# Performance work log

Measured on AMD Instinct MI355X. Metric: run time of the kernel, lower is better.

The kernel has to match this reference:

```python
import jax, jax.numpy as jnp
import numpy as np

N_NODES = 50000
K_MAX = 10
BATCH = 64
T = 32
N_INPUTS = 16
BITS_PER_FEATURE = 4
INPUT_BITS = N_INPUTS * BITS_PER_FEATURE  # 64


def setup_inputs() -> dict:
    key = jax.random.key(0)
    ks = jax.random.split(key, 8)
    x = jax.random.randint(ks[0], (BATCH, T, INPUT_BITS), 0, 2, dtype=jnp.int32)
    adj_list = jax.random.randint(ks[1], (N_NODES, K_MAX), 0, N_NODES, dtype=jnp.int32)
    adj_list_mask = jax.random.randint(ks[2], (N_NODES, K_MAX), 0, 2, dtype=jnp.int32)
    lut = jax.random.randint(ks[3], (N_NODES, 2 ** K_MAX), 0, 2, dtype=jnp.int32)
    init_states = jax.random.randint(ks[4], (N_NODES,), 0, 2, dtype=jnp.int32)
    input_nodes = jax.random.randint(ks[5], (INPUT_BITS,), 0, N_NODES, dtype=jnp.int32)
    W = jax.random.normal(ks[6], (N_INPUTS, N_NODES), dtype=jnp.float32) * (1.0 / np.sqrt(N_NODES))
    b = jax.random.normal(ks[7], (N_INPUTS,), dtype=jnp.float32) * 0.01
    return {"x": x, "adj_list": adj_list, "adj_list_mask": adj_list_mask,
            "lut": lut, "init_states": init_states, "input_nodes": input_nodes,
            "W": W, "b": b}


def reference(x, adj_list, adj_list_mask, lut, init_states, input_nodes, W, b):
    B, T_, _ = x.shape
    N, K = adj_list.shape
    # powers_of_2 = 2**arange(K).flip()  (MSB-first bit packing)
    pow2 = (2 ** jnp.arange(K - 1, -1, -1)).astype(jnp.int32)  # [K]
    node_ids = jnp.arange(N, dtype=jnp.int32)  # [N]
    s0 = jnp.broadcast_to(init_states[None, :], (B, N)).astype(jnp.int32)

    def step(states, x_t):
        # xor input perturbation at input_nodes
        cur = states[:, input_nodes]                      # [B, INPUT_BITS]
        states = states.at[:, input_nodes].set(jnp.bitwise_xor(cur, x_t))
        # gather masked neighbor states and bit-pack into LUT index
        neigh = jnp.take(states, adj_list, axis=1)        # [B, N, K]
        idx = jnp.sum(neigh * adj_list_mask[None] * pow2, axis=-1)  # [B, N]
        new_states = lut[node_ids[None, :], idx]          # [B, N]
        return new_states, None

    final_states, _ = jax.lax.scan(step, s0, jnp.moveaxis(x, 1, 0))
    # readout = nn.Linear(n_nodes, n_inputs) on final binary states
    out = final_states.astype(jnp.float32) @ W.T + b      # [B, N_INPUTS]
    return out
```

## Files before the change

### kernel.cpp

```cpp
#include <hip/hip_runtime.h>
#include <stdint.h>

#define N_NODES    50000
#define K_MAX      10
#define BATCH      64
#define T_STEPS    32
#define N_INPUTS   16
#define INPUT_BITS 64

#define NPW   224
#define NWG   224
#define NTHR  896
#define GRPN  14
#define GRP_SZ 16
#define NBUF  (T_STEPS + 1)

#define BUF_STRIDE_B 400128u

#define OFF_BUFS   0u
#define OFF_XMASK  13204224u
#define OFF_GCTR   13220608u
#define OFF_RCTR   13335296u
#define OFF_PLUT   13343488u

__global__ void prep_kernel(const int* __restrict__ x,
                            const int* __restrict__ init_states,
                            const int* __restrict__ input_nodes,
                            uint64_t* __restrict__ bufs,
                            uint64_t* __restrict__ xmask,
                            uint32_t* __restrict__ gctr,
                            uint32_t* __restrict__ rctr) {
    const int gid = blockIdx.x * blockDim.x + threadIdx.x;
    const size_t strw = BUF_STRIDE_B / 8;
    if (gid < N_NODES) {
        int n = gid;
        int jm = -1;
        for (int j = 0; j < INPUT_BITS; ++j)
            if (input_nodes[j] == n) jm = j;
        uint64_t v = init_states[n] ? ~0ull : 0ull;
        if (jm >= 0) {
            uint64_t m = 0ull;
            for (int b = 0; b < BATCH; ++b)
                m |= (uint64_t)(x[b * (T_STEPS * INPUT_BITS) + jm] & 1) << b;
            v ^= m;
        }
        bufs[n] = v;
    } else if (gid < N_NODES + NBUF) {
        bufs[(size_t)(gid - N_NODES) * strw + N_NODES] = 0ull;
    } else if (gid < N_NODES + NBUF + T_STEPS * INPUT_BITS) {
        int k = gid - (N_NODES + NBUF);
        int t = k >> 6, j = k & 63;
        uint64_t m = 0ull;
        for (int b = 0; b < BATCH; ++b)
            m |= (uint64_t)(x[b * (T_STEPS * INPUT_BITS) + t * INPUT_BITS + j] & 1) << b;
        xmask[k] = m;
    } else {
        int c = gid - (N_NODES + NBUF + T_STEPS * INPUT_BITS);
        if (c < T_STEPS * GRPN) gctr[c * 64] = 0;
        else if (c < T_STEPS * GRPN + T_STEPS)
            rctr[(c - T_STEPS * GRPN) * 64] = 0;
    }
}

__global__ void lutpack_kernel(const int* __restrict__ lut,
                               uint64_t* __restrict__ plut) {
    const int tid = threadIdx.x;
    const int blk = blockIdx.x;
    const int lane = tid & 63, wave = tid >> 6;
    int v = lut[(size_t)blk * 1024 + tid];
    uint64_t m = __ballot(v & 1);
    if (lane == 0) plut[(size_t)blk * 16 + wave] = m;
}

__global__ __launch_bounds__(NTHR)
void reservoir_coop(const uint64_t* __restrict__ plut,
                    const int* __restrict__ adj,
                    const int* __restrict__ adjmask,
                    const int* __restrict__ input_nodes,
                    const uint64_t* __restrict__ xmask,
                    uint64_t* __restrict__ bufs,
                    uint32_t* __restrict__ gctr,
                    uint32_t* __restrict__ rctr) {
    __shared__ uint8_t lutb[NPW * 128];

    const int tid = threadIdx.x;
    const int wg  = blockIdx.x;
    const int grp = wg >> 4;

    {
        const uint4* s = (const uint4*)(plut + (size_t)wg * NPW * 16);
        uint4* d = (uint4*)lutb;
        d[tid]        = s[tid];
        d[tid + NTHR] = s[tid + NTHR];
    }

    const int nl   = tid >> 2;
    const int q    = tid & 3;
    const int node = wg * NPW + nl;
    const bool valid = node < N_NODES;
    const uint32_t qsh = (uint32_t)(q & 1) * 16;

    uint32_t off[K_MAX];
    uint32_t soff = 0;
    int jm = -1;
    if (valid) {
        #pragma unroll
        for (int k = 0; k < K_MAX; ++k) {
            int a  = adj[node * K_MAX + k];
            int mk = adjmask[node * K_MAX + k];
            off[k] = (uint32_t)(mk ? a : N_NODES) * 8u + (uint32_t)(q >> 1) * 4u;
        }
        for (int j = 0; j < INPUT_BITS; ++j)
            if (input_nodes[j] == node) jm = j;
        soff = (uint32_t)node * 8u + (uint32_t)(q >> 1) * 4u;
    }
    const uint32_t* lut32 = (const uint32_t*)lutb;
    const uint32_t* xm32  = (const uint32_t*)xmask;
    const int rowbase = nl * 32;
    __syncthreads();

    for (int t = 0; t < T_STEPS; ++t) {
        const char* src = (const char*)bufs + (size_t)t * BUF_STRIDE_B;
        char*       dst = (char*)bufs + (size_t)(t + 1) * BUF_STRIDE_B;
        if (valid) {
            uint32_t w[K_MAX];
            #pragma unroll
            for (int k = 0; k < K_MAX; ++k)
                w[k] = *(const uint32_t*)(src + off[k]) >> qsh;

            uint32_t o16 = 0;
            #pragma unroll
            for (int b = 0; b < 16; ++b) {
                uint32_t idx = 0;
                #pragma unroll
                for (int k = 0; k < K_MAX; ++k)
                    idx = (idx << 1) | ((w[k] >> b) & 1u);
                uint32_t d = lut32[rowbase + (idx >> 5)];
                o16 |= ((d >> (idx & 31)) & 1u) << b;
            }

            uint32_t hi = __shfl_down(o16, 1);
            if ((q & 1) == 0) {
                uint32_t o32 = o16 | (hi << 16);
                if (jm >= 0 && t < T_STEPS - 1)
                    o32 ^= xm32[((t + 1) * INPUT_BITS + jm) * 2 + (q >> 1)];
                __hip_atomic_store((uint32_t*)(dst + soff), o32,
                                   __ATOMIC_RELAXED, __HIP_MEMORY_SCOPE_AGENT);
            }
        }

        if (t < T_STEPS - 1) {
            __syncthreads();
            if (tid == 0) {
                uint32_t* gc = gctr + ((size_t)t * GRPN + grp) * 64;
                uint32_t* rc = rctr + (size_t)t * 64;
                uint32_t old = __hip_atomic_fetch_add(gc, 1u, __ATOMIC_RELAXED,
                                                      __HIP_MEMORY_SCOPE_AGENT);
                if (old == GRP_SZ - 1)
                    __hip_atomic_fetch_add(rc, 1u, __ATOMIC_RELAXED,
                                           __HIP_MEMORY_SCOPE_AGENT);
                while (__hip_atomic_load(rc, __ATOMIC_RELAXED, __HIP_MEMORY_SCOPE_AGENT)
                       < (uint32_t)GRPN)
                    __builtin_amdgcn_s_sleep(1);
            }
            __syncthreads();
        }
    }
}

__global__ void out_kernel(const uint64_t* __restrict__ fstate,
                           const float* __restrict__ W,
                           const float* __restrict__ bias,
                           float* __restrict__ out) {
    const int wg = blockIdx.x;
    const int b = wg >> 4, i = wg & 15;
    const int tid = threadIdx.x;
    const uint8_t* st = (const uint8_t*)fstate;
    const int byteoff = b >> 3, bsh = b & 7;

    float s = 0.f;
    for (int n = tid; n < N_NODES; n += 256) {
        uint32_t bit = (st[(size_t)n * 8 + byteoff] >> bsh) & 1u;
        s += (float)bit * W[(size_t)i * N_NODES + n];
    }
    #pragma unroll
    for (int off = 32; off; off >>= 1) s += __shfl_down(s, off);

    __shared__ float part[4];
    const int lane = tid & 63, wave = tid >> 6;
    if (lane == 0) part[wave] = s;
    __syncthreads();
    if (tid == 0) out[wg] = part[0] + part[1] + part[2] + part[3] + bias[i];
}

extern "C" void kernel_launch(void* const* d_in, const int* in_sizes, int n_in,
                              void* d_out, int out_size, void* d_ws, size_t ws_size,
                              hipStream_t stream) {
    const int*   x       = (const int*)d_in[0];
    const int*   adj     = (const int*)d_in[1];
    const int*   adjmask = (const int*)d_in[2];
    const int*   lut     = (const int*)d_in[3];
    const int*   initst  = (const int*)d_in[4];
    const int*   innodes = (const int*)d_in[5];
    const float* W       = (const float*)d_in[6];
    const float* bias    = (const float*)d_in[7];
    float* out = (float*)d_out;

    char* ws = (char*)d_ws;
    uint64_t* bufs  = (uint64_t*)(ws + OFF_BUFS);
    uint64_t* xmask = (uint64_t*)(ws + OFF_XMASK);
    uint32_t* gctr  = (uint32_t*)(ws + OFF_GCTR);
    uint32_t* rctr  = (uint32_t*)(ws + OFF_RCTR);
    uint64_t* plut  = (uint64_t*)(ws + OFF_PLUT);

    {
        int prep_threads = N_NODES + NBUF + T_STEPS * INPUT_BITS
                         + T_STEPS * GRPN + T_STEPS;
        int prep_blocks = (prep_threads + 255) / 256;
        hipLaunchKernelGGL(prep_kernel, dim3(prep_blocks), dim3(256), 0, stream,
                           x, initst, innodes, bufs, xmask, gctr, rctr);
    }

    hipLaunchKernelGGL(lutpack_kernel, dim3(N_NODES), dim3(1024), 0, stream, lut, plut);

    {
        void* args[] = { (void*)&plut, (void*)&adj, (void*)&adjmask, (void*)&innodes,
                         (void*)&xmask, (void*)&bufs, (void*)&gctr, (void*)&rctr };
        hipLaunchCooperativeKernel((void*)reservoir_coop,
                                   dim3(NWG), dim3(NTHR),
                                   args, 0, stream);
    }

    hipLaunchKernelGGL(out_kernel, dim3(BATCH * N_INPUTS), dim3(256), 0, stream,
                       (const uint64_t*)(ws + OFF_BUFS + (size_t)T_STEPS * BUF_STRIDE_B),
                       W, bias, out);
}
```

Before: 365.0 us.

## Fuse LUT bit-packing into cooperative kernel and regrid to 512 smaller workgroups

Removes the separate lutpack kernel and its packed-LUT round trip through global memory. Each workgroup now ballots its own nodes' int32 LUT rows straight into shared memory. The cooperative grid changes from 224 workgroups of 896 threads to 512 of 448 threads, which spreads the one-time 200 MB LUT read across more CUs and raises the number of barrier groups. The cost is more participants in every per-step grid barrier. Threads beyond NPW now run the compute on dummy offsets and skip only the store.

After: 384.2 us. 5.3% more time.

```diff
diff --git a/kernel.cpp b/kernel.cpp
--- a/kernel.cpp
+++ b/kernel.cpp
@@ -8,10 +8,10 @@
 #define N_INPUTS   16
 #define INPUT_BITS 64
 
-#define NPW   224
-#define NWG   224
-#define NTHR  896
-#define GRPN  14
+#define NPW   98
+#define NWG   512
+#define NTHR  448
+#define GRPN  32
 #define GRP_SZ 16
 #define NBUF  (T_STEPS + 1)
 
@@ -20,8 +20,7 @@
 #define OFF_BUFS   0u
 #define OFF_XMASK  13204224u
 #define OFF_GCTR   13220608u
-#define OFF_RCTR   13335296u
-#define OFF_PLUT   13343488u
+#define OFF_RCTR   13482752u
 
 __global__ void prep_kernel(const int* __restrict__ x,
                             const int* __restrict__ init_states,
@@ -62,20 +61,10 @@
     }
 }
 
-__global__ void lutpack_kernel(const int* __restrict__ lut,
-                               uint64_t* __restrict__ plut) {
-    const int tid = threadIdx.x;
-    const int blk = blockIdx.x;
-    const int lane = tid & 63, wave = tid >> 6;
-    int v = lut[(size_t)blk * 1024 + tid];
-    uint64_t m = __ballot(v & 1);
-    if (lane == 0) plut[(size_t)blk * 16 + wave] = m;
-}
-
 __global__ __launch_bounds__(NTHR)
-void reservoir_coop(const uint64_t* __restrict__ plut,
-                    const int* __restrict__ adj,
+void reservoir_coop(const int* __restrict__ adj,
                     const int* __restrict__ adjmask,
+                    const int* __restrict__ lut,
                     const int* __restrict__ input_nodes,
                     const uint64_t* __restrict__ xmask,
                     uint64_t* __restrict__ bufs,
@@ -83,26 +72,39 @@
                     uint32_t* __restrict__ rctr) {
     __shared__ uint8_t lutb[NPW * 128];
 
-    const int tid = threadIdx.x;
-    const int wg  = blockIdx.x;
-    const int grp = wg >> 4;
-
-    {
-        const uint4* s = (const uint4*)(plut + (size_t)wg * NPW * 16);
-        uint4* d = (uint4*)lutb;
-        d[tid]        = s[tid];
-        d[tid + NTHR] = s[tid + NTHR];
+    const int tid  = threadIdx.x;
+    const int wg   = blockIdx.x;
+    const int grp  = wg >> 4;
+    const int lane = tid & 63;
+    const int wv   = tid >> 6;
+
+    for (int rr = 0; rr < 14; ++rr) {
+        int r  = wv * 14 + rr;
+        int gn = wg * NPW + r;
+        if (gn < N_NODES) {
+            uint64_t mine = 0ull;
+            #pragma unroll
+            for (int c = 0; c < 16; ++c) {
+                int v = lut[(size_t)gn * 1024 + (size_t)c * 64 + lane];
+                uint64_t m = __ballot(v & 1);
+                if (lane == c) mine = m;
+            }
+            if (lane < 16) ((uint64_t*)lutb)[r * 16 + lane] = mine;
+        }
     }
 
     const int nl   = tid >> 2;
     const int q    = tid & 3;
     const int node = wg * NPW + nl;
-    const bool valid = node < N_NODES;
+    const bool valid = (nl < NPW) && (node < N_NODES);
     const uint32_t qsh = (uint32_t)(q & 1) * 16;
 
     uint32_t off[K_MAX];
     uint32_t soff = 0;
     int jm = -1;
+    #pragma unroll
+    for (int k = 0; k < K_MAX; ++k)
+        off[k] = (uint32_t)N_NODES * 8u + (uint32_t)(q >> 1) * 4u;
     if (valid) {
         #pragma unroll
         for (int k = 0; k < K_MAX; ++k) {
@@ -122,31 +124,30 @@
     for (int t = 0; t < T_STEPS; ++t) {
         const char* src = (const char*)bufs + (size_t)t * BUF_STRIDE_B;
         char*       dst = (char*)bufs + (size_t)(t + 1) * BUF_STRIDE_B;
-        if (valid) {
-            uint32_t w[K_MAX];
+
+        uint32_t w[K_MAX];
+        #pragma unroll
+        for (int k = 0; k < K_MAX; ++k)
+            w[k] = *(const uint32_t*)(src + off[k]) >> qsh;
+
+        uint32_t o16 = 0;
+        #pragma unroll
+        for (int b = 0; b < 16; ++b) {
+            uint32_t idx = 0;
             #pragma unroll
             for (int k = 0; k < K_MAX; ++k)
-                w[k] = *(const uint32_t*)(src + off[k]) >> qsh;
-
-            uint32_t o16 = 0;
-            #pragma unroll
-            for (int b = 0; b < 16; ++b) {
-                uint32_t idx = 0;
-                #pragma unroll
-                for (int k = 0; k < K_MAX; ++k)
-                    idx = (idx << 1) | ((w[k] >> b) & 1u);
-                uint32_t d = lut32[rowbase + (idx >> 5)];
-                o16 |= ((d >> (idx & 31)) & 1u) << b;
-            }
-
-            uint32_t hi = __shfl_down(o16, 1);
-            if ((q & 1) == 0) {
-                uint32_t o32 = o16 | (hi << 16);
-                if (jm >= 0 && t < T_STEPS - 1)
-                    o32 ^= xm32[((t + 1) * INPUT_BITS + jm) * 2 + (q >> 1)];
-                __hip_atomic_store((uint32_t*)(dst + soff), o32,
-                                   __ATOMIC_RELAXED, __HIP_MEMORY_SCOPE_AGENT);
-            }
+                idx = (idx << 1) | ((w[k] >> b) & 1u);
+            uint32_t d = lut32[rowbase + (idx >> 5)];
+            o16 |= ((d >> (idx & 31)) & 1u) << b;
+        }
+
+        uint32_t hi16 = __shfl_down(o16, 1);
+        if (valid && (q & 1) == 0) {
+            uint32_t o32 = o16 | (hi16 << 16);
+            if (jm >= 0 && t < T_STEPS - 1)
+                o32 ^= xm32[((t + 1) * INPUT_BITS + jm) * 2 + (q >> 1)];
+            __hip_atomic_store((uint32_t*)(dst + soff), o32,
+                               __ATOMIC_RELAXED, __HIP_MEMORY_SCOPE_AGENT);
         }
 
         if (t < T_STEPS - 1) {
@@ -211,7 +212,6 @@
     uint64_t* xmask = (uint64_t*)(ws + OFF_XMASK);
     uint32_t* gctr  = (uint32_t*)(ws + OFF_GCTR);
     uint32_t* rctr  = (uint32_t*)(ws + OFF_RCTR);
-    uint64_t* plut  = (uint64_t*)(ws + OFF_PLUT);
 
     {
         int prep_threads = N_NODES + NBUF + T_STEPS * INPUT_BITS
@@ -221,10 +221,8 @@
                            x, initst, innodes, bufs, xmask, gctr, rctr);
     }
 
-    hipLaunchKernelGGL(lutpack_kernel, dim3(N_NODES), dim3(1024), 0, stream, lut, plut);
-
     {
-        void* args[] = { (void*)&plut, (void*)&adj, (void*)&adjmask, (void*)&innodes,
+        void* args[] = { (void*)&adj, (void*)&adjmask, (void*)&lut, (void*)&innodes,
                          (void*)&xmask, (void*)&bufs, (void*)&gctr, (void*)&rctr };
         hipLaunchCooperativeKernel((void*)reservoir_coop,
                                    dim3(NWG), dim3(NTHR),
```
